# Optimization experiments

Measured on AMD Instinct MI355X. Metric: run time of the kernel, lower is better.

## Reference

```python
import jax, jax.numpy as jnp
import numpy as np

B, T, C = 4, 2048, 1024
N_HEAD = 16
HEAD_DIM = C // N_HEAD


def setup_inputs() -> dict:
    key = jax.random.key(0)
    k1, k2, k3 = jax.random.split(key, 3)
    scale = 0.02
    x = jax.random.normal(k1, (B, T, C), dtype=jnp.float32)
    W_attn = jax.random.normal(k2, (C, 3 * C), dtype=jnp.float32) * scale
    b_attn = jnp.zeros((3 * C,), dtype=jnp.float32)
    W_proj = jax.random.normal(k3, (C, C), dtype=jnp.float32) * scale
    b_proj = jnp.zeros((C,), dtype=jnp.float32)
    return {"x": x, "W_attn": W_attn, "b_attn": b_attn, "W_proj": W_proj, "b_proj": b_proj}


def reference(x, W_attn, b_attn, W_proj, b_proj):
    Bx, Tx, Cx = x.shape
    qkv = x @ W_attn + b_attn                      # [B,T,3C]
    q, k, v = jnp.split(qkv, 3, axis=-1)
    def split_heads(t):
        return t.reshape(Bx, Tx, N_HEAD, HEAD_DIM).transpose(0, 2, 1, 3)  # [B,H,T,D]
    q, k, v = split_heads(q), split_heads(k), split_heads(v)
    att = jnp.einsum('bhqd,bhkd->bhqk', q, k) / jnp.sqrt(jnp.float32(HEAD_DIM))
    causal = jnp.tril(jnp.ones((Tx, Tx), dtype=bool))
    att = jnp.where(causal, att, jnp.float32(-jnp.inf))
    att = jax.nn.softmax(att, axis=-1)
    y = jnp.einsum('bhqk,bhkd->bhqd', att, v)      # [B,H,T,D]
    y = y.transpose(0, 2, 1, 3).reshape(Bx, Tx, Cx)
    return y @ W_proj + b_proj
```

## Files before the change

### kernel.cpp

```cpp
#include <hip/hip_runtime.h>
#include <hip/hip_bf16.h>
#include <math.h>

#define B_  4
#define T_  2048
#define C_  1024
#define NH  16
#define HD  64
#define M_  (B_ * T_)
#define N_QKV (3 * C_)
#define KDIM 1024
#define SCALE2 0.18033688011112042f

typedef __attribute__((ext_vector_type(8))) short short8;
typedef __attribute__((ext_vector_type(4))) short bs4;
typedef __attribute__((ext_vector_type(4))) float f32x4;
typedef __attribute__((ext_vector_type(16))) float f32x16;
typedef __attribute__((ext_vector_type(4))) unsigned u32x4;

__device__ __forceinline__ short f2bs(float f) {
  __hip_bfloat16 h = __float2bfloat16(f);
  return *reinterpret_cast<short*>(&h);
}
__device__ __forceinline__ unsigned pack2(float a, float b) {
  return (unsigned)(unsigned short)f2bs(a) | ((unsigned)(unsigned short)f2bs(b) << 16);
}

__device__ __forceinline__ void gload16(const void* g, void* l) {
  __builtin_amdgcn_global_load_lds(
      (const __attribute__((address_space(1))) void*)g,
      (__attribute__((address_space(3))) void*)l, 16, 0, 0);
}

__global__ __launch_bounds__(256) void wtrans_kernel(
    const float* __restrict__ W, short* __restrict__ Wt, int Ncols)
{
  __shared__ short t[32][33];
  const int nb = Ncols / 32;
  const int bn = blockIdx.x % nb, bk = blockIdx.x / nb;
  const int tid = threadIdx.x;
  const int r = tid >> 3, c4 = (tid & 7) * 4;
  f32x4 v = *reinterpret_cast<const f32x4*>(
      W + (size_t)(bk * 32 + r) * Ncols + bn * 32 + c4);
  #pragma unroll
  for (int j = 0; j < 4; ++j) t[r][c4 + j] = f2bs(v[j]);
  __syncthreads();
  bs4 o;
  #pragma unroll
  for (int j = 0; j < 4; ++j) o[j] = t[c4 + j][r];
  *reinterpret_cast<bs4*>(Wt + (size_t)(bn * 32 + r) * KDIM + bk * 32 + c4) = o;
}

template<bool A_BF16, bool OUT_BF16>
__global__ __launch_bounds__(256) void gemm128_kernel(
    const void* __restrict__ Aptr, const short* __restrict__ Bt,
    const float* __restrict__ bias, void* __restrict__ outptr, int N)
{
  __shared__ short As[128 * 32];
  __shared__ short Bs[128 * 32];

  const int tid  = threadIdx.x;
  const int lane = tid & 63;
  const int w    = tid >> 6;
  const int wr   = w >> 1, wc = w & 1;
  const int rl   = lane & 15, kg = lane >> 4;
  const int nblk = N >> 7;
  const int m0 = (blockIdx.x / nblk) << 7;
  const int n0 = (blockIdx.x % nblk) << 7;

  f32x4 acc[4][4] = {};

  const int srow = w * 32 + (lane >> 2);
  const int scol = ((lane & 3) ^ ((lane >> 3) & 3)) * 8;
  const short* pb0 = Bt + (size_t)(n0 + srow) * KDIM + scol;
  const short* pb1 = pb0 + (size_t)16 * KDIM;
  short* const lb0 = &Bs[w * 1024];
  short* const lb1 = &Bs[w * 1024 + 512];

  const short* pa0 = nullptr; const short* pa1 = nullptr;
  short* la0 = nullptr; short* la1 = nullptr;
  const float* paf = nullptr; short* lafA = nullptr; short* lafB = nullptr;
  if constexpr (A_BF16) {
    pa0 = (const short*)Aptr + (size_t)(m0 + srow) * KDIM + scol;
    pa1 = pa0 + (size_t)16 * KDIM;
    la0 = &As[w * 1024];
    la1 = &As[w * 1024 + 512];
  } else {
    const int arow  = w * 32 + (lane >> 1);
    const int half  = lane & 1;
    const int phase = (lane >> 2) & 3;
    paf  = (const float*)Aptr + (size_t)(m0 + arow) * KDIM + half * 16;
    lafA = &As[arow * 32 + ((2 * half)     ^ phase) * 8];
    lafB = &As[arow * 32 + ((2 * half + 1) ^ phase) * 8];
  }

  const int sread = (kg ^ ((rl >> 1) & 3)) * 8;

  for (int k0 = 0; k0 < KDIM; k0 += 32) {
    __syncthreads();
    if constexpr (A_BF16) {
      gload16(pa0 + k0, la0);
      gload16(pa1 + k0, la1);
    } else {
      const float* p = paf + k0;
      f32x4 f0 = *reinterpret_cast<const f32x4*>(p);
      f32x4 f1 = *reinterpret_cast<const f32x4*>(p + 4);
      f32x4 f2 = *reinterpret_cast<const f32x4*>(p + 8);
      f32x4 f3 = *reinterpret_cast<const f32x4*>(p + 12);
      short8 lo, hi;
      #pragma unroll
      for (int j = 0; j < 4; ++j) {
        lo[j] = f2bs(f0[j]); lo[4 + j] = f2bs(f1[j]);
        hi[j] = f2bs(f2[j]); hi[4 + j] = f2bs(f3[j]);
      }
      *reinterpret_cast<short8*>(lafA) = lo;
      *reinterpret_cast<short8*>(lafB) = hi;
    }
    gload16(pb0 + k0, lb0);
    gload16(pb1 + k0, lb1);
    __syncthreads();

    short8 af[4], bf[4];
    #pragma unroll
    for (int i = 0; i < 4; ++i) {
      af[i] = *reinterpret_cast<short8*>(&As[(wr * 64 + i * 16 + rl) * 32 + sread]);
      bf[i] = *reinterpret_cast<short8*>(&Bs[(wc * 64 + i * 16 + rl) * 32 + sread]);
    }
    #pragma unroll
    for (int mi = 0; mi < 4; ++mi)
      #pragma unroll
      for (int ni = 0; ni < 4; ++ni)
        acc[mi][ni] = __builtin_amdgcn_mfma_f32_16x16x32_bf16(
            af[mi], bf[ni], acc[mi][ni], 0, 0, 0);
  }

  #pragma unroll
  for (int ni = 0; ni < 4; ++ni) {
    const int col = n0 + wc * 64 + ni * 16 + rl;
    const float bv = bias[col];
    #pragma unroll
    for (int mi = 0; mi < 4; ++mi) {
      #pragma unroll
      for (int r = 0; r < 4; ++r) {
        const int row = m0 + wr * 64 + mi * 16 + kg * 4 + r;
        const float v = acc[mi][ni][r] + bv;
        if constexpr (OUT_BF16)
          ((short*)outptr)[(size_t)row * N + col] = f2bs(v);
        else
          ((float*)outptr)[(size_t)row * N + col] = v;
      }
    }
  }
}

__global__ __launch_bounds__(256) void attn_mfma3_kernel(
    const short* __restrict__ qkv, short* __restrict__ y)
{
  __shared__ short Ks[2][64 * 64];
  __shared__ short Vt[2][64 * 64];

  const int tid  = threadIdx.x;
  const int lane = tid & 63;
  const int w    = tid >> 6;
  const int q32  = lane & 31;
  const int hi   = lane >> 5;

  const int bid  = blockIdx.x;
  const int pair = bid >> 6;
  const int bh   = bid & 63;
  const int b    = bh >> 4, h = bh & 15;
  const size_t bT = (size_t)b * T_;

  const int kr0 = tid >> 3;
  const int kl0 = (tid & 7) ^ ((tid >> 3) & 7);
  const int kr1 = (tid + 256) >> 3;
  const int kl1 = (tid & 7) ^ (((tid + 256) >> 3) & 7);
  const size_t kbase0 = (bT + kr0) * N_QKV + C_ + h * HD + kl0 * 8;
  const size_t kbase1 = (bT + kr1) * N_QKV + C_ + h * HD + kl1 * 8;
  short* const kdst0 = &Ks[0][(w * 64) * 8];
  short* const kdst1 = &Ks[0][(w * 64 + 256) * 8];

  const int vkey = tid & 63;
  const int vd16 = (tid >> 6) * 16;
  const size_t vbase = (bT + vkey) * N_QKV + 2 * C_ + h * HD + vd16;

  const int ksl = q32 & 7;

  #pragma unroll 1
  for (int sel = 0; sel < 2; ++sel) {
    const int qi  = sel ? (15 - pair) : pair;
    const int nkb = 2 * qi + 2;
    const int wq0 = qi * 128 + w * 32;
    const int q   = wq0 + q32;

    short8 qf[4];
    #pragma unroll
    for (int kd = 0; kd < 4; ++kd)
      qf[kd] = *reinterpret_cast<const short8*>(
          qkv + (bT + q) * N_QKV + h * HD + kd * 16 + hi * 8);

    f32x16 o0 = {}, o1 = {};
    float m_ = -INFINITY, l_ = 0.f;

    {
      gload16(qkv + kbase0, kdst0);
      gload16(qkv + kbase1, kdst1);
      short8 va = *reinterpret_cast<const short8*>(qkv + vbase);
      short8 vb = *reinterpret_cast<const short8*>(qkv + vbase + 8);
      #pragma unroll
      for (int j = 0; j < 8; ++j) {
        Vt[0][(vd16 + j) * 64 + (((vkey >> 3) ^ j) << 3) + (vkey & 7)]     = va[j];
        Vt[0][(vd16 + 8 + j) * 64 + (((vkey >> 3) ^ j) << 3) + (vkey & 7)] = vb[j];
      }
    }
    __syncthreads();

    int cur = 0;
    for (int kb = 0; kb < nkb; ++kb) {
      const bool more = (kb + 1 < nkb);
      short8 va, vb;
      if (more) {
        const size_t koff = (size_t)(kb + 1) * 64 * N_QKV;
        gload16(qkv + kbase0 + koff, kdst0 + (cur ^ 1) * 4096);
        gload16(qkv + kbase1 + koff, kdst1 + (cur ^ 1) * 4096);
        va = *reinterpret_cast<const short8*>(qkv + vbase + koff);
        vb = *reinterpret_cast<const short8*>(qkv + vbase + koff + 8);
      }

      const int kmin = kb * 64;
      if (kmin <= wq0 + 31) {
        const short* ksc = &Ks[cur][0];
        const short* vtc = &Vt[cur][0];

        f32x16 s0 = {}, s1 = {};
        #pragma unroll
        for (int kd = 0; kd < 4; ++kd) {
          const int sl = ((2 * kd + hi) ^ ksl) * 8;
          short8 kf0 = *reinterpret_cast<const short8*>(&ksc[q32 * 64 + sl]);
          short8 kf1 = *reinterpret_cast<const short8*>(&ksc[(32 + q32) * 64 + sl]);
          s0 = __builtin_amdgcn_mfma_f32_32x32x16_bf16(kf0, qf[kd], s0, 0, 0, 0);
          s1 = __builtin_amdgcn_mfma_f32_32x32x16_bf16(kf1, qf[kd], s1, 0, 0, 0);
        }

        const bool needmask = (kmin + 63 > wq0);
        if (needmask) {
          const int qrel = q - kmin - 4 * hi;
          #pragma unroll
          for (int e = 0; e < 16; ++e) {
            const int ko = (e & 3) + 8 * (e >> 2);
            s0[e] = (ko > qrel)      ? -INFINITY : s0[e] * SCALE2;
            s1[e] = (ko + 32 > qrel) ? -INFINITY : s1[e] * SCALE2;
          }
        } else {
          #pragma unroll
          for (int e = 0; e < 16; ++e) { s0[e] *= SCALE2; s1[e] *= SCALE2; }
        }

        float mx = s0[0];
        #pragma unroll
        for (int e = 1; e < 16; ++e) mx = fmaxf(mx, s0[e]);
        #pragma unroll
        for (int e = 0; e < 16; ++e) mx = fmaxf(mx, s1[e]);
        mx = fmaxf(mx, __shfl_xor(mx, 32, 64));
        const float mn = fmaxf(m_, mx);
        const float cr = exp2f(m_ - mn);
        m_ = mn;
        float rs = 0.f;
        #pragma unroll
        for (int e = 0; e < 16; ++e) {
          s0[e] = exp2f(s0[e] - mn); rs += s0[e];
          s1[e] = exp2f(s1[e] - mn); rs += s1[e];
        }
        rs += __shfl_xor(rs, 32, 64);
        l_ = l_ * cr + rs;
        #pragma unroll
        for (int e = 0; e < 16; ++e) { o0[e] *= cr; o1[e] *= cr; }

        unsigned pk[2][4][2], sw[2][4][2];
        #pragma unroll
        for (int g = 0; g < 4; ++g)
          #pragma unroll
          for (int p = 0; p < 2; ++p) {
            pk[0][g][p] = pack2(s0[4 * g + 2 * p], s0[4 * g + 2 * p + 1]);
            pk[1][g][p] = pack2(s1[4 * g + 2 * p], s1[4 * g + 2 * p + 1]);
            sw[0][g][p] = (unsigned)__shfl_xor((int)pk[0][g][p], 32, 64);
            sw[1][g][p] = (unsigned)__shfl_xor((int)pk[1][g][p], 32, 64);
          }

        #pragma unroll
        for (int kk = 0; kk < 4; ++kk) {
          const int c = kk >> 1, a2 = 2 * (kk & 1);
          u32x4 t;
          t[0] = hi ? sw[c][a2 + 1][0] : pk[c][a2][0];
          t[1] = hi ? sw[c][a2 + 1][1] : pk[c][a2][1];
          t[2] = hi ? pk[c][a2 + 1][0] : sw[c][a2][0];
          t[3] = hi ? pk[c][a2 + 1][1] : sw[c][a2][1];
          const short8 pb = __builtin_bit_cast(short8, t);
          const int sl = ((2 * kk + hi) ^ ksl) * 8;
          short8 vf0 = *reinterpret_cast<const short8*>(&vtc[q32 * 64 + sl]);
          short8 vf1 = *reinterpret_cast<const short8*>(&vtc[(32 + q32) * 64 + sl]);
          o0 = __builtin_amdgcn_mfma_f32_32x32x16_bf16(vf0, pb, o0, 0, 0, 0);
          o1 = __builtin_amdgcn_mfma_f32_32x32x16_bf16(vf1, pb, o1, 0, 0, 0);
        }
      }

      if (more) {
        #pragma unroll
        for (int j = 0; j < 8; ++j) {
          Vt[cur ^ 1][(vd16 + j) * 64 + (((vkey >> 3) ^ j) << 3) + (vkey & 7)]     = va[j];
          Vt[cur ^ 1][(vd16 + 8 + j) * 64 + (((vkey >> 3) ^ j) << 3) + (vkey & 7)] = vb[j];
        }
      }
      __syncthreads();
      cur ^= 1;
    }

    const float inv = 1.f / l_;
    short* const yp = y + (bT + q) * C_ + h * HD;
    #pragma unroll
    for (int g = 0; g < 4; ++g) {
      bs4 ov0, ov1;
      #pragma unroll
      for (int t = 0; t < 4; ++t) {
        ov0[t] = f2bs(o0[4 * g + t] * inv);
        ov1[t] = f2bs(o1[4 * g + t] * inv);
      }
      *reinterpret_cast<bs4*>(yp + 8 * g + 4 * hi)      = ov0;
      *reinterpret_cast<bs4*>(yp + 32 + 8 * g + 4 * hi) = ov1;
    }
  }
}

extern "C" void kernel_launch(void* const* d_in, const int* in_sizes, int n_in,
                              void* d_out, int out_size, void* d_ws, size_t ws_size,
                              hipStream_t stream) {
  const float* x  = (const float*)d_in[0];
  const float* Wa = (const float*)d_in[1];
  const float* ba = (const float*)d_in[2];
  const float* Wp = (const float*)d_in[3];
  const float* bp = (const float*)d_in[4];

  short* qkvb = (short*)d_ws;
  short* yb   = qkvb + (size_t)M_ * N_QKV;
  short* WaT  = yb + (size_t)M_ * C_;
  short* WpT  = WaT;

  wtrans_kernel<<<(KDIM / 32) * (N_QKV / 32), 256, 0, stream>>>(Wa, WaT, N_QKV);
  gemm128_kernel<false, true><<<(M_ / 128) * (N_QKV / 128), 256, 0, stream>>>(
      x, WaT, ba, qkvb, N_QKV);
  wtrans_kernel<<<(KDIM / 32) * (C_ / 32), 256, 0, stream>>>(Wp, WpT, C_);
  attn_mfma3_kernel<<<8 * B_ * NH, 256, 0, stream>>>(qkvb, yb);
  gemm128_kernel<true, false><<<(M_ / 128) * (C_ / 128), 256, 0, stream>>>(
      yb, WpT, bp, d_out, C_);
}
```

Measured before the change: 235.4 us.

## Fold softmax scale into Q weights, lazy rescale, one q-tile per block

The softmax scale (1/sqrt(d)·log2e) is folded into the Q columns of the transposed QKV weight and bias, so the attention kernel no longer multiplies every score. The online softmax now rescales the running max and accumulators only when some lane's block max exceeds the old max by more than 8 (in log2 units), which skips most rescale work. The grid doubles so each block handles one 128-row query tile instead of a balanced pair, with the longest tiles launched first. The lazy threshold lets exponentials reach up to 2^8 before bf16 packing, and the unpaired tiles can leave the load less evenly balanced.

```diff
diff --git a/kernel.cpp b/kernel.cpp
--- a/kernel.cpp
+++ b/kernel.cpp
@@ -33,17 +33,18 @@
 }
 
 __global__ __launch_bounds__(256) void wtrans_kernel(
-    const float* __restrict__ W, short* __restrict__ Wt, int Ncols)
+    const float* __restrict__ W, short* __restrict__ Wt, int Ncols, int qcols)
 {
   __shared__ short t[32][33];
   const int nb = Ncols / 32;
   const int bn = blockIdx.x % nb, bk = blockIdx.x / nb;
   const int tid = threadIdx.x;
   const int r = tid >> 3, c4 = (tid & 7) * 4;
+  const float cs = (bn * 32 < qcols) ? SCALE2 : 1.f;
   f32x4 v = *reinterpret_cast<const f32x4*>(
       W + (size_t)(bk * 32 + r) * Ncols + bn * 32 + c4);
   #pragma unroll
-  for (int j = 0; j < 4; ++j) t[r][c4 + j] = f2bs(v[j]);
+  for (int j = 0; j < 4; ++j) t[r][c4 + j] = f2bs(v[j] * cs);
   __syncthreads();
   bs4 o;
   #pragma unroll
@@ -54,7 +55,7 @@
 template<bool A_BF16, bool OUT_BF16>
 __global__ __launch_bounds__(256) void gemm128_kernel(
     const void* __restrict__ Aptr, const short* __restrict__ Bt,
-    const float* __restrict__ bias, void* __restrict__ outptr, int N)
+    const float* __restrict__ bias, void* __restrict__ outptr, int N, int nq)
 {
   __shared__ short As[128 * 32];
   __shared__ short Bs[128 * 32];
@@ -137,7 +138,8 @@
   #pragma unroll
   for (int ni = 0; ni < 4; ++ni) {
     const int col = n0 + wc * 64 + ni * 16 + rl;
-    const float bv = bias[col];
+    float bv = bias[col];
+    if (col < nq) bv *= SCALE2;
     #pragma unroll
     for (int mi = 0; mi < 4; ++mi) {
       #pragma unroll
@@ -153,7 +155,7 @@
   }
 }
 
-__global__ __launch_bounds__(256) void attn_mfma3_kernel(
+__global__ __launch_bounds__(256) void attn_mfma4_kernel(
     const short* __restrict__ qkv, short* __restrict__ y)
 {
   __shared__ short Ks[2][64 * 64];
@@ -166,7 +168,7 @@
   const int hi   = lane >> 5;
 
   const int bid  = blockIdx.x;
-  const int pair = bid >> 6;
+  const int qi   = 15 - (bid >> 6);
   const int bh   = bid & 63;
   const int b    = bh >> 4, h = bh & 15;
   const size_t bT = (size_t)b * T_;
@@ -186,148 +188,145 @@
 
   const int ksl = q32 & 7;
 
-  #pragma unroll 1
-  for (int sel = 0; sel < 2; ++sel) {
-    const int qi  = sel ? (15 - pair) : pair;
-    const int nkb = 2 * qi + 2;
-    const int wq0 = qi * 128 + w * 32;
-    const int q   = wq0 + q32;
-
-    short8 qf[4];
-    #pragma unroll
-    for (int kd = 0; kd < 4; ++kd)
-      qf[kd] = *reinterpret_cast<const short8*>(
-          qkv + (bT + q) * N_QKV + h * HD + kd * 16 + hi * 8);
-
-    f32x16 o0 = {}, o1 = {};
-    float m_ = -INFINITY, l_ = 0.f;
-
-    {
-      gload16(qkv + kbase0, kdst0);
-      gload16(qkv + kbase1, kdst1);
-      short8 va = *reinterpret_cast<const short8*>(qkv + vbase);
-      short8 vb = *reinterpret_cast<const short8*>(qkv + vbase + 8);
-      #pragma unroll
-      for (int j = 0; j < 8; ++j) {
-        Vt[0][(vd16 + j) * 64 + (((vkey >> 3) ^ j) << 3) + (vkey & 7)]     = va[j];
-        Vt[0][(vd16 + 8 + j) * 64 + (((vkey >> 3) ^ j) << 3) + (vkey & 7)] = vb[j];
-      }
-    }
-    __syncthreads();
-
-    int cur = 0;
-    for (int kb = 0; kb < nkb; ++kb) {
-      const bool more = (kb + 1 < nkb);
-      short8 va, vb;
-      if (more) {
-        const size_t koff = (size_t)(kb + 1) * 64 * N_QKV;
-        gload16(qkv + kbase0 + koff, kdst0 + (cur ^ 1) * 4096);
-        gload16(qkv + kbase1 + koff, kdst1 + (cur ^ 1) * 4096);
-        va = *reinterpret_cast<const short8*>(qkv + vbase + koff);
-        vb = *reinterpret_cast<const short8*>(qkv + vbase + koff + 8);
-      }
-
-      const int kmin = kb * 64;
-      if (kmin <= wq0 + 31) {
-        const short* ksc = &Ks[cur][0];
-        const short* vtc = &Vt[cur][0];
-
-        f32x16 s0 = {}, s1 = {};
+  const int nkb = 2 * qi + 2;
+  const int wq0 = qi * 128 + w * 32;
+  const int q   = wq0 + q32;
+
+  short8 qf[4];
+  #pragma unroll
+  for (int kd = 0; kd < 4; ++kd)
+    qf[kd] = *reinterpret_cast<const short8*>(
+        qkv + (bT + q) * N_QKV + h * HD + kd * 16 + hi * 8);
+
+  f32x16 o0 = {}, o1 = {};
+  float m_ = -INFINITY, l_ = 0.f;
+
+  {
+    gload16(qkv + kbase0, kdst0);
+    gload16(qkv + kbase1, kdst1);
+    short8 va = *reinterpret_cast<const short8*>(qkv + vbase);
+    short8 vb = *reinterpret_cast<const short8*>(qkv + vbase + 8);
+    #pragma unroll
+    for (int j = 0; j < 8; ++j) {
+      Vt[0][(vd16 + j) * 64 + (((vkey >> 3) ^ j) << 3) + (vkey & 7)]     = va[j];
+      Vt[0][(vd16 + 8 + j) * 64 + (((vkey >> 3) ^ j) << 3) + (vkey & 7)] = vb[j];
+    }
+  }
+  __syncthreads();
+
+  int cur = 0;
+  for (int kb = 0; kb < nkb; ++kb) {
+    const bool more = (kb + 1 < nkb);
+    short8 va, vb;
+    if (more) {
+      const size_t koff = (size_t)(kb + 1) * 64 * N_QKV;
+      gload16(qkv + kbase0 + koff, kdst0 + (cur ^ 1) * 4096);
+      gload16(qkv + kbase1 + koff, kdst1 + (cur ^ 1) * 4096);
+      va = *reinterpret_cast<const short8*>(qkv + vbase + koff);
+      vb = *reinterpret_cast<const short8*>(qkv + vbase + koff + 8);
+    }
+
+    const int kmin = kb * 64;
+    if (kmin <= wq0 + 31) {
+      const short* ksc = &Ks[cur][0];
+      const short* vtc = &Vt[cur][0];
+
+      f32x16 s0 = {}, s1 = {};
+      #pragma unroll
+      for (int kd = 0; kd < 4; ++kd) {
+        const int sl = ((2 * kd + hi) ^ ksl) * 8;
+        short8 kf0 = *reinterpret_cast<const short8*>(&ksc[q32 * 64 + sl]);
+        short8 kf1 = *reinterpret_cast<const short8*>(&ksc[(32 + q32) * 64 + sl]);
+        s0 = __builtin_amdgcn_mfma_f32_32x32x16_bf16(kf0, qf[kd], s0, 0, 0, 0);
+        s1 = __builtin_amdgcn_mfma_f32_32x32x16_bf16(kf1, qf[kd], s1, 0, 0, 0);
+      }
+
+      if (kmin + 63 > wq0) {
+        const int qrel = q - kmin - 4 * hi;
         #pragma unroll
-        for (int kd = 0; kd < 4; ++kd) {
-          const int sl = ((2 * kd + hi) ^ ksl) * 8;
-          short8 kf0 = *reinterpret_cast<const short8*>(&ksc[q32 * 64 + sl]);
-          short8 kf1 = *reinterpret_cast<const short8*>(&ksc[(32 + q32) * 64 + sl]);
-          s0 = __builtin_amdgcn_mfma_f32_32x32x16_bf16(kf0, qf[kd], s0, 0, 0, 0);
-          s1 = __builtin_amdgcn_mfma_f32_32x32x16_bf16(kf1, qf[kd], s1, 0, 0, 0);
+        for (int e = 0; e < 16; ++e) {
+          const int ko = (e & 3) + 8 * (e >> 2);
+          if (ko > qrel)      s0[e] = -INFINITY;
+          if (ko + 32 > qrel) s1[e] = -INFINITY;
         }
-
-        const bool needmask = (kmin + 63 > wq0);
-        if (needmask) {
-          const int qrel = q - kmin - 4 * hi;
-          #pragma unroll
-          for (int e = 0; e < 16; ++e) {
-            const int ko = (e & 3) + 8 * (e >> 2);
-            s0[e] = (ko > qrel)      ? -INFINITY : s0[e] * SCALE2;
-            s1[e] = (ko + 32 > qrel) ? -INFINITY : s1[e] * SCALE2;
-          }
-        } else {
-          #pragma unroll
-          for (int e = 0; e < 16; ++e) { s0[e] *= SCALE2; s1[e] *= SCALE2; }
-        }
-
-        float mx = s0[0];
-        #pragma unroll
-        for (int e = 1; e < 16; ++e) mx = fmaxf(mx, s0[e]);
-        #pragma unroll
-        for (int e = 0; e < 16; ++e) mx = fmaxf(mx, s1[e]);
-        mx = fmaxf(mx, __shfl_xor(mx, 32, 64));
+      }
+
+      float mx = s0[0];
+      #pragma unroll
+      for (int e = 1; e < 16; ++e) mx = fmaxf(mx, s0[e]);
+      #pragma unroll
+      for (int e = 0; e < 16; ++e) mx = fmaxf(mx, s1[e]);
+      mx = fmaxf(mx, __shfl_xor(mx, 32, 64));
+
+      if (!__all(mx <= m_ + 8.f)) {
         const float mn = fmaxf(m_, mx);
         const float cr = exp2f(m_ - mn);
         m_ = mn;
-        float rs = 0.f;
-        #pragma unroll
-        for (int e = 0; e < 16; ++e) {
-          s0[e] = exp2f(s0[e] - mn); rs += s0[e];
-          s1[e] = exp2f(s1[e] - mn); rs += s1[e];
-        }
-        rs += __shfl_xor(rs, 32, 64);
-        l_ = l_ * cr + rs;
+        l_ *= cr;
         #pragma unroll
         for (int e = 0; e < 16; ++e) { o0[e] *= cr; o1[e] *= cr; }
-
-        unsigned pk[2][4][2], sw[2][4][2];
+      }
+
+      float rs = 0.f;
+      #pragma unroll
+      for (int e = 0; e < 16; ++e) {
+        s0[e] = exp2f(s0[e] - m_); rs += s0[e];
+        s1[e] = exp2f(s1[e] - m_); rs += s1[e];
+      }
+      rs += __shfl_xor(rs, 32, 64);
+      l_ += rs;
+
+      unsigned pk[2][4][2], sw[2][4][2];
+      #pragma unroll
+      for (int g = 0; g < 4; ++g)
         #pragma unroll
-        for (int g = 0; g < 4; ++g)
-          #pragma unroll
-          for (int p = 0; p < 2; ++p) {
-            pk[0][g][p] = pack2(s0[4 * g + 2 * p], s0[4 * g + 2 * p + 1]);
-            pk[1][g][p] = pack2(s1[4 * g + 2 * p], s1[4 * g + 2 * p + 1]);
-            sw[0][g][p] = (unsigned)__shfl_xor((int)pk[0][g][p], 32, 64);
-            sw[1][g][p] = (unsigned)__shfl_xor((int)pk[1][g][p], 32, 64);
-          }
-
-        #pragma unroll
-        for (int kk = 0; kk < 4; ++kk) {
-          const int c = kk >> 1, a2 = 2 * (kk & 1);
-          u32x4 t;
-          t[0] = hi ? sw[c][a2 + 1][0] : pk[c][a2][0];
-          t[1] = hi ? sw[c][a2 + 1][1] : pk[c][a2][1];
-          t[2] = hi ? pk[c][a2 + 1][0] : sw[c][a2][0];
-          t[3] = hi ? pk[c][a2 + 1][1] : sw[c][a2][1];
-          const short8 pb = __builtin_bit_cast(short8, t);
-          const int sl = ((2 * kk + hi) ^ ksl) * 8;
-          short8 vf0 = *reinterpret_cast<const short8*>(&vtc[q32 * 64 + sl]);
-          short8 vf1 = *reinterpret_cast<const short8*>(&vtc[(32 + q32) * 64 + sl]);
-          o0 = __builtin_amdgcn_mfma_f32_32x32x16_bf16(vf0, pb, o0, 0, 0, 0);
-          o1 = __builtin_amdgcn_mfma_f32_32x32x16_bf16(vf1, pb, o1, 0, 0, 0);
+        for (int p = 0; p < 2; ++p) {
+          pk[0][g][p] = pack2(s0[4 * g + 2 * p], s0[4 * g + 2 * p + 1]);
+          pk[1][g][p] = pack2(s1[4 * g + 2 * p], s1[4 * g + 2 * p + 1]);
+          sw[0][g][p] = (unsigned)__shfl_xor((int)pk[0][g][p], 32, 64);
+          sw[1][g][p] = (unsigned)__shfl_xor((int)pk[1][g][p], 32, 64);
         }
-      }
-
-      if (more) {
-        #pragma unroll
-        for (int j = 0; j < 8; ++j) {
-          Vt[cur ^ 1][(vd16 + j) * 64 + (((vkey >> 3) ^ j) << 3) + (vkey & 7)]     = va[j];
-          Vt[cur ^ 1][(vd16 + 8 + j) * 64 + (((vkey >> 3) ^ j) << 3) + (vkey & 7)] = vb[j];
-        }
-      }
-      __syncthreads();
-      cur ^= 1;
-    }
-
-    const float inv = 1.f / l_;
-    short* const yp = y + (bT + q) * C_ + h * HD;
-    #pragma unroll
-    for (int g = 0; g < 4; ++g) {
-      bs4 ov0, ov1;
-      #pragma unroll
-      for (int t = 0; t < 4; ++t) {
-        ov0[t] = f2bs(o0[4 * g + t] * inv);
-        ov1[t] = f2bs(o1[4 * g + t] * inv);
-      }
-      *reinterpret_cast<bs4*>(yp + 8 * g + 4 * hi)      = ov0;
-      *reinterpret_cast<bs4*>(yp + 32 + 8 * g + 4 * hi) = ov1;
-    }
+
+      #pragma unroll
+      for (int kk = 0; kk < 4; ++kk) {
+        const int c = kk >> 1, a2 = 2 * (kk & 1);
+        u32x4 t;
+        t[0] = hi ? sw[c][a2 + 1][0] : pk[c][a2][0];
+        t[1] = hi ? sw[c][a2 + 1][1] : pk[c][a2][1];
+        t[2] = hi ? pk[c][a2 + 1][0] : sw[c][a2][0];
+        t[3] = hi ? pk[c][a2 + 1][1] : sw[c][a2][1];
+        const short8 pb = __builtin_bit_cast(short8, t);
+        const int sl = ((2 * kk + hi) ^ ksl) * 8;
+        short8 vf0 = *reinterpret_cast<const short8*>(&vtc[q32 * 64 + sl]);
+        short8 vf1 = *reinterpret_cast<const short8*>(&vtc[(32 + q32) * 64 + sl]);
+        o0 = __builtin_amdgcn_mfma_f32_32x32x16_bf16(vf0, pb, o0, 0, 0, 0);
+        o1 = __builtin_amdgcn_mfma_f32_32x32x16_bf16(vf1, pb, o1, 0, 0, 0);
+      }
+    }
+
+    if (more) {
+      #pragma unroll
+      for (int j = 0; j < 8; ++j) {
+        Vt[cur ^ 1][(vd16 + j) * 64 + (((vkey >> 3) ^ j) << 3) + (vkey & 7)]     = va[j];
+        Vt[cur ^ 1][(vd16 + 8 + j) * 64 + (((vkey >> 3) ^ j) << 3) + (vkey & 7)] = vb[j];
+      }
+    }
+    __syncthreads();
+    cur ^= 1;
+  }
+
+  const float inv = 1.f / l_;
+  short* const yp = y + (bT + q) * C_ + h * HD;
+  #pragma unroll
+  for (int g = 0; g < 4; ++g) {
+    bs4 ov0, ov1;
+    #pragma unroll
+    for (int t = 0; t < 4; ++t) {
+      ov0[t] = f2bs(o0[4 * g + t] * inv);
+      ov1[t] = f2bs(o1[4 * g + t] * inv);
+    }
+    *reinterpret_cast<bs4*>(yp + 8 * g + 4 * hi)      = ov0;
+    *reinterpret_cast<bs4*>(yp + 32 + 8 * g + 4 * hi) = ov1;
   }
 }
 
@@ -345,11 +344,11 @@
   short* WaT  = yb + (size_t)M_ * C_;
   short* WpT  = WaT;
 
-  wtrans_kernel<<<(KDIM / 32) * (N_QKV / 32), 256, 0, stream>>>(Wa, WaT, N_QKV);
+  wtrans_kernel<<<(KDIM / 32) * (N_QKV / 32), 256, 0, stream>>>(Wa, WaT, N_QKV, C_);
   gemm128_kernel<false, true><<<(M_ / 128) * (N_QKV / 128), 256, 0, stream>>>(
-      x, WaT, ba, qkvb, N_QKV);
-  wtrans_kernel<<<(KDIM / 32) * (C_ / 32), 256, 0, stream>>>(Wp, WpT, C_);
-  attn_mfma3_kernel<<<8 * B_ * NH, 256, 0, stream>>>(qkvb, yb);
+      x, WaT, ba, qkvb, N_QKV, C_);
+  wtrans_kernel<<<(KDIM / 32) * (C_ / 32), 256, 0, stream>>>(Wp, WpT, C_, 0);
+  attn_mfma4_kernel<<<16 * B_ * NH, 256, 0, stream>>>(qkvb, yb);
   gemm128_kernel<true, false><<<(M_ / 128) * (C_ / 128), 256, 0, stream>>>(
-      yb, WpT, bp, d_out, C_);
-}
+      yb, WpT, bp, d_out, C_, 0);
+}
```

Result: faster. 229.0 us (-2.7%).
